# Optimization experiments

Measured on AMD Instinct MI355X. Metric: run time of the kernel, lower is better.

## Reference

```python
import jax, jax.numpy as jnp
import numpy as np

DIM = 256
HEADS = 4
DEPTH = DIM // HEADS
EXPAND = 4
EPS = 1e-3  # keras BatchNormalization default epsilon


def _bn(x, gamma, beta, mean, var):
    # inference-mode batch norm over last axis
    return gamma * (x - mean) * jax.lax.rsqrt(var + EPS) + beta


def setup_inputs() -> dict:
    key = jax.random.key(0)
    ks = jax.random.split(key, 12)
    B, S, D = 4, 2048, DIM
    H = D * EXPAND
    s = 1.0 / np.sqrt(D)
    inp = {
        "x": jax.random.normal(ks[0], (B, S, D), jnp.float32),
        "bn1_gamma": jnp.ones((D,), jnp.float32),
        "bn1_beta": jnp.zeros((D,), jnp.float32),
        "bn1_mean": jax.random.normal(ks[1], (D,), jnp.float32) * 0.1,
        "bn1_var": jnp.abs(jax.random.normal(ks[2], (D,), jnp.float32)) + 0.5,
        "wq": jax.random.normal(ks[3], (D, D), jnp.float32) * s,
        "bq": jnp.zeros((D,), jnp.float32),
        "wk": jax.random.normal(ks[4], (D, D), jnp.float32) * s,
        "bk": jnp.zeros((D,), jnp.float32),
        "wv": jax.random.normal(ks[5], (D, D), jnp.float32) * s,
        "bv": jnp.zeros((D,), jnp.float32),
        "wo": jax.random.normal(ks[6], (D, D), jnp.float32) * s,
        "bo": jnp.zeros((D,), jnp.float32),
        "bn2_gamma": jnp.ones((D,), jnp.float32),
        "bn2_beta": jnp.zeros((D,), jnp.float32),
        "bn2_mean": jax.random.normal(ks[7], (D,), jnp.float32) * 0.1,
        "bn2_var": jnp.abs(jax.random.normal(ks[8], (D,), jnp.float32)) + 0.5,
        "w1": jax.random.normal(ks[9], (D, H), jnp.float32) * s,
        "w2": jax.random.normal(ks[10], (H, D), jnp.float32) * (1.0 / np.sqrt(H)),
    }
    return inp


def reference(x, bn1_gamma, bn1_beta, bn1_mean, bn1_var,
              wq, bq, wk, bk, wv, bv, wo, bo,
              bn2_gamma, bn2_beta, bn2_mean, bn2_var, w1, w2):
    B, S, D = x.shape
    h = _bn(x, bn1_gamma, bn1_beta, bn1_mean, bn1_var)
    # project and split heads -> [B, H, S, depth]
    def heads(t):
        return t.reshape(B, S, HEADS, DEPTH).transpose(0, 2, 1, 3)
    q = heads(h @ wq + bq)
    k = heads(h @ wk + bk)
    v = heads(h @ wv + bv)
    scores = jnp.einsum("bhqd,bhkd->bhqk", q, k) / jnp.sqrt(jnp.float32(DEPTH))
    attn = jax.nn.softmax(scores, axis=-1)
    ctx = jnp.einsum("bhqk,bhkd->bhqd", attn, v)
    ctx = ctx.transpose(0, 2, 1, 3).reshape(B, S, D)
    attn_out = ctx @ wo + bo
    x1 = attn_out + x  # residual (dropout = identity at inference)
    h2 = _bn(x1, bn2_gamma, bn2_beta, bn2_mean, bn2_var)
    m = jax.nn.gelu(h2 @ w1, approximate=False) @ w2
    return m + x1
```

## Files before the change

### kernel.cpp

```cpp
#include <hip/hip_runtime.h>

typedef unsigned short u16;
typedef unsigned int u32;
typedef short short8 __attribute__((ext_vector_type(8)));
typedef float f32x4 __attribute__((ext_vector_type(4)));

#define EPS 1e-3f
#define C1F 0.18033688011112042f

static __device__ __forceinline__ u16 f2bf(float f) {
    u32 u = __float_as_uint(f);
    u += 0x7fffu + ((u >> 16) & 1u);
    return (u16)(u >> 16);
}
static __device__ __forceinline__ u32 pack_bf2(float a, float b) {
    u32 ua = __float_as_uint(a) + 0x8000u;
    u32 ub = __float_as_uint(b) + 0x8000u;
    return __builtin_amdgcn_perm(ub, ua, 0x07060302u);
}
static __device__ __forceinline__ void async_cp16(const void* g, void* l) {
    __builtin_amdgcn_global_load_lds(
        (const __attribute__((address_space(1))) unsigned int*)g,
        (__attribute__((address_space(3))) unsigned int*)l, 16, 0, 0);
}

__global__ void prep_kernel(const float* __restrict__ wq, const float* __restrict__ wk,
                            const float* __restrict__ wv, const float* __restrict__ wo,
                            const float* __restrict__ w1, const float* __restrict__ w2,
                            const float* __restrict__ bq, const float* __restrict__ bk,
                            const float* __restrict__ g1, const float* __restrict__ b1,
                            const float* __restrict__ m1, const float* __restrict__ v1,
                            const float* __restrict__ g2, const float* __restrict__ b2,
                            const float* __restrict__ m2, const float* __restrict__ v2,
                            u16* __restrict__ wqkT, u16* __restrict__ wvT,
                            u16* __restrict__ woT, u16* __restrict__ w1T,
                            u16* __restrict__ w2T, float* __restrict__ bqk,
                            float* __restrict__ bn1sc, float* __restrict__ bn1sh,
                            float* __restrict__ bn2sc, float* __restrict__ bn2sh) {
    int idx = blockIdx.x * 256 + threadIdx.x;
    if (idx < 131072) {
        int n = idx >> 8, k = idx & 255;
        float v = (n < 256) ? wq[k * 256 + n] : wk[k * 256 + (n - 256)] * C1F;
        wqkT[idx] = f2bf(v);
    } else if (idx < 196608) {
        int i = idx - 131072; int n = i >> 8, k = i & 255;
        wvT[i] = f2bf(wv[k * 256 + n]);
    } else if (idx < 262144) {
        int i = idx - 196608; int n = i >> 8, k = i & 255;
        woT[i] = f2bf(wo[k * 256 + n]);
    } else if (idx < 524288) {
        int i = idx - 262144; int n = i >> 8, k = i & 255;
        w1T[i] = f2bf(w1[k * 1024 + n]);
    } else if (idx < 786432) {
        int i = idx - 524288; int n = i >> 10, k = i & 1023;
        w2T[i] = f2bf(w2[k * 256 + n]);
    } else if (idx < 786944) {
        int i = idx - 786432;
        bqk[i] = (i < 256) ? bq[i] : bk[i - 256] * C1F;
    } else if (idx < 787200) {
        int i = idx - 786944;
        float sc = g1[i] * rsqrtf(v1[i] + EPS);
        bn1sc[i] = sc; bn1sh[i] = b1[i] - m1[i] * sc;
    } else if (idx < 787456) {
        int i = idx - 787200;
        float sc = g2[i] * rsqrtf(v2[i] + EPS);
        bn2sc[i] = sc; bn2sh[i] = b2[i] - m2[i] * sc;
    }
}

__global__ void bn1_kernel(const float* __restrict__ x, const float* __restrict__ sc,
                           const float* __restrict__ sh, u16* __restrict__ h) {
    int idx = blockIdx.x * 256 + threadIdx.x;
    int base = idx * 4;
    int c = base & 255;
    float4 xv = *(const float4*)(x + base);
    float4 s4 = *(const float4*)(sc + c);
    float4 h4 = *(const float4*)(sh + c);
    ushort4 pk;
    pk.x = f2bf(fmaf(xv.x, s4.x, h4.x));
    pk.y = f2bf(fmaf(xv.y, s4.y, h4.y));
    pk.z = f2bf(fmaf(xv.z, s4.z, h4.z));
    pk.w = f2bf(fmaf(xv.w, s4.w, h4.w));
    *(ushort4*)(h + base) = pk;
}

template <int EPI, int MT>
__global__ __launch_bounds__(256) void gemm_ws(
        const u16* __restrict__ A, const u16* __restrict__ Bt,
        int M, int N, int K,
        const float* __restrict__ bias, const float* __restrict__ resid,
        float* __restrict__ out_f32, u16* __restrict__ out_bf,
        const float* __restrict__ b2sc, const float* __restrict__ b2sh) {
    __shared__ u16 lds_b[64 * 256];
    const int t = threadIdx.x;
    const int w = t >> 6, lane = t & 63;
    const int l = lane & 15, Q = lane >> 4;
    const int m0 = blockIdx.x * (MT * 64);
    const int n0 = blockIdx.y * 64;

    f32x4 acc[MT][4];
#pragma unroll
    for (int mt = 0; mt < MT; ++mt)
#pragma unroll
        for (int nt = 0; nt < 4; ++nt) acc[mt][nt] = (f32x4){0.f, 0.f, 0.f, 0.f};

    for (int kc = 0; kc < K; kc += 256) {
        __syncthreads();
#pragma unroll
        for (int j = 0; j < 8; ++j) {
            int cw = (w * 8 + j) * 64 + lane;
            int r = cw >> 5;
            int cs = cw & 31;
            int c = (cs & 24) | ((cs & 7) ^ (r & 7));
            async_cp16(Bt + (size_t)(n0 + r) * K + kc + c * 8, (char*)lds_b + (w * 8 + j) * 1024);
        }
        __syncthreads();
#pragma unroll
        for (int kd = 0; kd < 8; ++kd) {
            short8 bfr[4];
#pragma unroll
            for (int nt = 0; nt < 4; ++nt) {
                int r = nt * 16 + l;
                int c = kd * 4 + Q;
                int slot = (c & 24) | ((c & 7) ^ (r & 7));
                bfr[nt] = *(const short8*)(lds_b + r * 256 + slot * 8);
            }
#pragma unroll
            for (int mt = 0; mt < MT; ++mt) {
                short8 afr = *(const short8*)(A + (size_t)(m0 + w * 16 * MT + mt * 16 + l) * K
                                              + kc + kd * 32 + Q * 8);
#pragma unroll
                for (int nt = 0; nt < 4; ++nt)
                    acc[mt][nt] = __builtin_amdgcn_mfma_f32_16x16x32_bf16(afr, bfr[nt], acc[mt][nt], 0, 0, 0);
            }
        }
    }

#pragma unroll
    for (int mt = 0; mt < MT; ++mt)
#pragma unroll
        for (int nt = 0; nt < 4; ++nt)
#pragma unroll
            for (int r = 0; r < 4; ++r) {
                int row = m0 + w * 16 * MT + mt * 16 + Q * 4 + r;
                int col = n0 + nt * 16 + l;
                float val = acc[mt][nt][r];
                size_t oidx = (size_t)row * N + col;
                if (EPI == 0) {
                    out_bf[oidx] = f2bf(val + bias[col]);
                } else if (EPI == 1) {
                    val += bias[col] + resid[oidx];
                    out_f32[oidx] = val;
                    out_bf[oidx] = f2bf(fmaf(val, b2sc[col], b2sh[col]));
                } else if (EPI == 2) {
                    float gl = 0.5f * val * (1.f + erff(val * 0.70710678118654752f));
                    out_bf[oidx] = f2bf(gl);
                } else {
                    out_f32[oidx] = val + resid[oidx];
                }
            }
}

__global__ __launch_bounds__(256) void gemm_bt4(
        const u16* __restrict__ A, const u16* __restrict__ Bt,
        int M, int N, int K,
        const float* __restrict__ bias, u16* __restrict__ out_bf) {
    __shared__ u16 lds_a[64][72];
    __shared__ u16 lds_b[64][72];
    const int t = threadIdx.x;
    const int wave = t >> 6, lane = t & 63;
    const int l = lane & 15, Q = lane >> 4;
    const int m0 = blockIdx.x * 64;
    const int n0 = blockIdx.y * 64;

    f32x4 acc[4];
#pragma unroll
    for (int nt = 0; nt < 4; ++nt) acc[nt] = (f32x4){0.f, 0.f, 0.f, 0.f};

    for (int k0 = 0; k0 < K; k0 += 64) {
        __syncthreads();
#pragma unroll
        for (int i = 0; i < 2; ++i) {
            int c = t + i * 256;
            int row = c >> 3, c8 = c & 7;
            *(uint4*)(&lds_a[row][c8 * 8]) =
                *(const uint4*)(A + (size_t)(m0 + row) * K + k0 + c8 * 8);
            *(uint4*)(&lds_b[row][c8 * 8]) =
                *(const uint4*)(Bt + (size_t)(n0 + row) * K + k0 + c8 * 8);
        }
        __syncthreads();
#pragma unroll
        for (int kd = 0; kd < 2; ++kd) {
            short8 afr = *(const short8*)(&lds_a[wave * 16 + l][kd * 32 + Q * 8]);
            short8 bfr[4];
#pragma unroll
            for (int nt = 0; nt < 4; ++nt)
                bfr[nt] = *(const short8*)(&lds_b[nt * 16 + l][kd * 32 + Q * 8]);
#pragma unroll
            for (int nt = 0; nt < 4; ++nt)
                acc[nt] = __builtin_amdgcn_mfma_f32_16x16x32_bf16(afr, bfr[nt], acc[nt], 0, 0, 0);
        }
    }
#pragma unroll
    for (int nt = 0; nt < 4; ++nt)
#pragma unroll
        for (int r = 0; r < 4; ++r) {
            int row = m0 + wave * 16 + Q * 4 + r;
            int col = n0 + nt * 16 + l;
            out_bf[(size_t)row * N + col] = f2bf(acc[nt][r] + bias[row]);
        }
}

static __device__ __forceinline__ void stage_tiles(const u16* kglob, const u16* vglob,
                                                   u16* kdst, u16* vdst,
                                                   int w, int lane, int kt) {
#pragma unroll
    for (int j = 0; j < 2; ++j) {
        int cw = (w * 2 + j) * 64 + lane;
        int r = cw >> 3;
        int c = (cw & 7) ^ (r & 7);
        async_cp16(kglob + ((size_t)(kt * 64 + r)) * 512 + c * 8, kdst + (w * 2 + j) * 512);
        async_cp16(vglob + ((size_t)r) * 8192 + kt * 64 + c * 8, vdst + (w * 2 + j) * 512);
    }
}

__global__ __launch_bounds__(256) void attn_kernel(const u16* __restrict__ qk,
                                                   const u16* __restrict__ vT,
                                                   float* __restrict__ opart,
                                                   float* __restrict__ lpart) {
    __shared__ u16 kbuf[2][4096];
    __shared__ u16 vbuf[2][4096];
    __shared__ u32 pbuf[8 * 16 * 36];
    const int t = threadIdx.x;
    const int w = t >> 6, lane = t & 63;
    const int l = lane & 15, Q = lane >> 4;
    const int qt = blockIdx.x;
    const int bh = blockIdx.y;
    const int sp = blockIdx.z;
    const int bb = bh >> 2, hd = bh & 3;
    const size_t rowbase = (size_t)bb * 2048;
    const int q0 = qt * 128 + w * 32;
    const int s_base = sp * 1024;

    short8 qf[2][2];
#pragma unroll
    for (int qg = 0; qg < 2; ++qg)
#pragma unroll
        for (int kd = 0; kd < 2; ++kd)
            qf[qg][kd] = *(const short8*)(qk + (rowbase + q0 + qg * 16 + l) * 512
                                          + hd * 64 + kd * 32 + Q * 8);

    f32x4 o[2][4];
#pragma unroll
    for (int qg = 0; qg < 2; ++qg)
#pragma unroll
        for (int dt = 0; dt < 4; ++dt) o[qg][dt] = (f32x4){0.f, 0.f, 0.f, 0.f};
    float lacc[2] = {0.f, 0.f};

    const u16* kglob = qk + (rowbase + s_base) * 512 + 256 + hd * 64;
    const u16* vglob = vT + ((size_t)(hd * 64)) * 8192 + rowbase + s_base;
    u32* pw = pbuf + w * 1152;

    stage_tiles(kglob, vglob, kbuf[0], vbuf[0], w, lane, 0);

    for (int kt = 0; kt < 16; ++kt) {
        __syncthreads();
        if (kt < 15)
            stage_tiles(kglob, vglob, kbuf[(kt + 1) & 1], vbuf[(kt + 1) & 1], w, lane, kt + 1);
        const u16* kb = kbuf[kt & 1];
        const u16* vb = vbuf[kt & 1];

#pragma unroll
        for (int st = 0; st < 4; ++st) {
            int r = st * 16 + l;
            short8 kf0 = *(const short8*)(kb + r * 64 + ((0 + Q) ^ (r & 7)) * 8);
            short8 kf1 = *(const short8*)(kb + r * 64 + ((4 + Q) ^ (r & 7)) * 8);
#pragma unroll
            for (int qg = 0; qg < 2; ++qg) {
                f32x4 s = (f32x4){0.f, 0.f, 0.f, 0.f};
                s = __builtin_amdgcn_mfma_f32_16x16x32_bf16(kf0, qf[qg][0], s, 0, 0, 0);
                s = __builtin_amdgcn_mfma_f32_16x16x32_bf16(kf1, qf[qg][1], s, 0, 0, 0);
                float p0 = exp2f(fminf(s[0], 100.f));
                float p1 = exp2f(fminf(s[1], 100.f));
                float p2 = exp2f(fminf(s[2], 100.f));
                float p3 = exp2f(fminf(s[3], 100.f));
                lacc[qg] += (p0 + p1) + (p2 + p3);
                u32 d0 = pack_bf2(p0, p1);
                u32 d1 = pack_bf2(p2, p3);
                *(uint2*)&pw[qg * 576 + l * 36 + st * 8 + Q * 2] = make_uint2(d0, d1);
            }
        }

#pragma unroll
        for (int cc = 0; cc < 2; ++cc) {
            short8 pf0 = *(const short8*)&pw[l * 36 + cc * 16 + Q * 4];
            short8 pf1 = *(const short8*)&pw[576 + l * 36 + cc * 16 + Q * 4];
#pragma unroll
            for (int dt = 0; dt < 4; ++dt) {
                int r = dt * 16 + l;
                short8 vf = *(const short8*)(vb + r * 64 + ((cc * 4 + Q) ^ (r & 7)) * 8);
                o[0][dt] = __builtin_amdgcn_mfma_f32_16x16x32_bf16(vf, pf0, o[0][dt], 0, 0, 0);
                o[1][dt] = __builtin_amdgcn_mfma_f32_16x16x32_bf16(vf, pf1, o[1][dt], 0, 0, 0);
            }
        }
    }

#pragma unroll
    for (int qg = 0; qg < 2; ++qg) {
        float v = lacc[qg];
        v += __shfl_xor(v, 16);
        v += __shfl_xor(v, 32);
        lacc[qg] = v;
    }
    float* ob = opart + (((size_t)sp * 16 + bh) * 2048 + q0) * 64;
#pragma unroll
    for (int qg = 0; qg < 2; ++qg)
#pragma unroll
        for (int dt = 0; dt < 4; ++dt)
            *(f32x4*)(ob + (size_t)(qg * 16 + l) * 64 + dt * 16 + Q * 4) = o[qg][dt];
    if (Q == 0) {
        size_t lb = ((size_t)sp * 16 + bh) * 2048 + q0;
        lpart[lb + l] = lacc[0];
        lpart[lb + 16 + l] = lacc[1];
    }
}

__global__ void combine_kernel(const float* __restrict__ opart,
                               const float* __restrict__ lpart,
                               u16* __restrict__ ctx) {
    int idx = blockIdx.x * 256 + threadIdx.x;
    int e = idx * 4;
    int row = e >> 8, col = e & 255;
    int b = row >> 11, s = row & 2047, h = col >> 6, d = col & 63;
    size_t pb = (((size_t)(b * 4 + h)) * 2048 + s) * 64 + d;
    f32x4 o1 = *(const f32x4*)(opart + pb);
    f32x4 o2 = *(const f32x4*)(opart + 2097152 + pb);
    size_t lb = (size_t)(b * 4 + h) * 2048 + s;
    float li = 1.0f / (lpart[lb] + lpart[32768 + lb]);
    ushort4 pk;
    pk.x = f2bf((o1[0] + o2[0]) * li);
    pk.y = f2bf((o1[1] + o2[1]) * li);
    pk.z = f2bf((o1[2] + o2[2]) * li);
    pk.w = f2bf((o1[3] + o2[3]) * li);
    *(ushort4*)(ctx + e) = pk;
}

extern "C" void kernel_launch(void* const* d_in, const int* in_sizes, int n_in,
                              void* d_out, int out_size, void* d_ws, size_t ws_size,
                              hipStream_t stream) {
    (void)in_sizes; (void)n_in; (void)out_size; (void)ws_size;
    const float* x  = (const float*)d_in[0];
    const float* g1 = (const float*)d_in[1];
    const float* b1 = (const float*)d_in[2];
    const float* m1 = (const float*)d_in[3];
    const float* v1 = (const float*)d_in[4];
    const float* wq = (const float*)d_in[5];
    const float* bq = (const float*)d_in[6];
    const float* wk = (const float*)d_in[7];
    const float* bk = (const float*)d_in[8];
    const float* wv = (const float*)d_in[9];
    const float* bv = (const float*)d_in[10];
    const float* wo = (const float*)d_in[11];
    const float* bo = (const float*)d_in[12];
    const float* g2 = (const float*)d_in[13];
    const float* b2 = (const float*)d_in[14];
    const float* m2 = (const float*)d_in[15];
    const float* v2 = (const float*)d_in[16];
    const float* w1 = (const float*)d_in[17];
    const float* w2 = (const float*)d_in[18];

    char* ws = (char*)d_ws;
    u16*   qkb   = (u16*)(ws + 0);
    u16*   ctxh  = (u16*)(ws + 8388608);
    float* x1    = (float*)(ws + 12582912);
    u16*   h2    = (u16*)(ws + 20971520);
    float* opart = (float*)(ws + 25165824);
    u16*   gbuf  = (u16*)(ws + 25165824);
    u16*   vTb   = (u16*)(ws + 41943040);
    u16*   wqkT  = (u16*)(ws + 46137344);
    u16*   wvT   = (u16*)(ws + 46399488);
    u16*   woT   = (u16*)(ws + 46530560);
    u16*   w1T   = (u16*)(ws + 46661632);
    u16*   w2T   = (u16*)(ws + 47185920);
    float* bqk   = (float*)(ws + 47710208);
    float* bn1sc = (float*)(ws + 47712256);
    float* bn1sh = (float*)(ws + 47713280);
    float* bn2sc = (float*)(ws + 47714304);
    float* bn2sh = (float*)(ws + 47715328);
    float* lpart = (float*)(ws + 12582912);
    u16*   h_buf = ctxh;
    u16*   ctx   = ctxh;
    float* out   = (float*)d_out;

    prep_kernel<<<3076, 256, 0, stream>>>(wq, wk, wv, wo, w1, w2, bq, bk,
                                          g1, b1, m1, v1, g2, b2, m2, v2,
                                          wqkT, wvT, woT, w1T, w2T, bqk,
                                          bn1sc, bn1sh, bn2sc, bn2sh);
    bn1_kernel<<<2048, 256, 0, stream>>>(x, bn1sc, bn1sh, h_buf);
    gemm_ws<0, 2><<<dim3(64, 8), 256, 0, stream>>>(
        h_buf, wqkT, 8192, 512, 256, bqk, nullptr, nullptr, qkb, nullptr, nullptr);
    gemm_bt4<<<dim3(4, 128), 256, 0, stream>>>(wvT, h_buf, 256, 8192, 256, bv, vTb);
    attn_kernel<<<dim3(16, 16, 2), 256, 0, stream>>>(qkb, vTb, opart, lpart);
    combine_kernel<<<2048, 256, 0, stream>>>(opart, lpart, ctx);
    gemm_ws<1, 1><<<dim3(128, 4), 256, 0, stream>>>(
        ctx, woT, 8192, 256, 256, bo, x, x1, h2, bn2sc, bn2sh);
    gemm_ws<2, 2><<<dim3(64, 16), 256, 0, stream>>>(
        h2, w1T, 8192, 1024, 256, nullptr, nullptr, nullptr, gbuf, nullptr, nullptr);
    gemm_ws<3, 1><<<dim3(128, 4), 256, 0, stream>>>(
        gbuf, w2T, 8192, 256, 1024, nullptr, x1, out, nullptr, nullptr, nullptr);
}
```

Measured before the change: 211.1 us.

## Fuse QKV projection, drop LDS in GEMMs, register-resident P, 4-way KV split

Merges the V projection into the QK GEMM, whose epilogue writes V transposed, so the separate gemm_bt4 launch is removed. GEMMs now load B fragments straight from global memory instead of staging them in LDS, which removes the barriers but may lose data reuse across waves. The attention kernel keeps softmax probabilities in registers and feeds them to 16x16x16 MFMAs instead of round-tripping through LDS. The KV split grows from 2 to 4 for more parallelism, with bf16 partial outputs that halve combine traffic at some precision cost.

```diff
diff --git a/kernel.cpp b/kernel.cpp
--- a/kernel.cpp
+++ b/kernel.cpp
@@ -3,16 +3,27 @@
 typedef unsigned short u16;
 typedef unsigned int u32;
 typedef short short8 __attribute__((ext_vector_type(8)));
+typedef short short4v __attribute__((ext_vector_type(4)));
 typedef float f32x4 __attribute__((ext_vector_type(4)));
 
 #define EPS 1e-3f
 #define C1F 0.18033688011112042f
+
+#if defined(__HIP_DEVICE_COMPILE__)
+#define MFMA16(a, b, c) __builtin_amdgcn_mfma_f32_16x16x16bf16_1k(a, b, c, 0, 0, 0)
+#else
+#define MFMA16(a, b, c) (c)
+#endif
 
 static __device__ __forceinline__ u16 f2bf(float f) {
     u32 u = __float_as_uint(f);
     u += 0x7fffu + ((u >> 16) & 1u);
     return (u16)(u >> 16);
 }
+static __device__ __forceinline__ float bf2f(u16 v) {
+    u32 u = (u32)v << 16;
+    return __uint_as_float(u);
+}
 static __device__ __forceinline__ u32 pack_bf2(float a, float b) {
     u32 ua = __float_as_uint(a) + 0x8000u;
     u32 ub = __float_as_uint(b) + 0x8000u;
@@ -28,23 +39,24 @@
                             const float* __restrict__ wv, const float* __restrict__ wo,
                             const float* __restrict__ w1, const float* __restrict__ w2,
                             const float* __restrict__ bq, const float* __restrict__ bk,
+                            const float* __restrict__ bv,
                             const float* __restrict__ g1, const float* __restrict__ b1,
                             const float* __restrict__ m1, const float* __restrict__ v1,
                             const float* __restrict__ g2, const float* __restrict__ b2,
                             const float* __restrict__ m2, const float* __restrict__ v2,
-                            u16* __restrict__ wqkT, u16* __restrict__ wvT,
-                            u16* __restrict__ woT, u16* __restrict__ w1T,
-                            u16* __restrict__ w2T, float* __restrict__ bqk,
+                            u16* __restrict__ wqkvT, u16* __restrict__ woT,
+                            u16* __restrict__ w1T, u16* __restrict__ w2T,
+                            float* __restrict__ bqkv,
                             float* __restrict__ bn1sc, float* __restrict__ bn1sh,
                             float* __restrict__ bn2sc, float* __restrict__ bn2sh) {
     int idx = blockIdx.x * 256 + threadIdx.x;
-    if (idx < 131072) {
+    if (idx < 196608) {
         int n = idx >> 8, k = idx & 255;
-        float v = (n < 256) ? wq[k * 256 + n] : wk[k * 256 + (n - 256)] * C1F;
-        wqkT[idx] = f2bf(v);
-    } else if (idx < 196608) {
-        int i = idx - 131072; int n = i >> 8, k = i & 255;
-        wvT[i] = f2bf(wv[k * 256 + n]);
+        float v;
+        if (n < 256)      v = wq[k * 256 + n];
+        else if (n < 512) v = wk[k * 256 + (n - 256)] * C1F;
+        else              v = wv[k * 256 + (n - 512)];
+        wqkvT[idx] = f2bf(v);
     } else if (idx < 262144) {
         int i = idx - 196608; int n = i >> 8, k = i & 255;
         woT[i] = f2bf(wo[k * 256 + n]);
@@ -54,15 +66,15 @@
     } else if (idx < 786432) {
         int i = idx - 524288; int n = i >> 10, k = i & 1023;
         w2T[i] = f2bf(w2[k * 256 + n]);
-    } else if (idx < 786944) {
+    } else if (idx < 787200) {
         int i = idx - 786432;
-        bqk[i] = (i < 256) ? bq[i] : bk[i - 256] * C1F;
-    } else if (idx < 787200) {
-        int i = idx - 786944;
+        bqkv[i] = (i < 256) ? bq[i] : (i < 512 ? bk[i - 256] * C1F : bv[i - 512]);
+    } else if (idx < 787456) {
+        int i = idx - 787200;
         float sc = g1[i] * rsqrtf(v1[i] + EPS);
         bn1sc[i] = sc; bn1sh[i] = b1[i] - m1[i] * sc;
-    } else if (idx < 787456) {
-        int i = idx - 787200;
+    } else if (idx < 787712) {
+        int i = idx - 787456;
         float sc = g2[i] * rsqrtf(v2[i] + EPS);
         bn2sc[i] = sc; bn2sh[i] = b2[i] - m2[i] * sc;
     }
@@ -85,129 +97,82 @@
 }
 
 template <int EPI, int MT>
-__global__ __launch_bounds__(256) void gemm_ws(
+__global__ __launch_bounds__(256) void gemm_nb(
         const u16* __restrict__ A, const u16* __restrict__ Bt,
         int M, int N, int K,
         const float* __restrict__ bias, const float* __restrict__ resid,
         float* __restrict__ out_f32, u16* __restrict__ out_bf,
+        u16* __restrict__ out_vt,
         const float* __restrict__ b2sc, const float* __restrict__ b2sh) {
-    __shared__ u16 lds_b[64 * 256];
     const int t = threadIdx.x;
     const int w = t >> 6, lane = t & 63;
     const int l = lane & 15, Q = lane >> 4;
-    const int m0 = blockIdx.x * (MT * 64);
+    const int m0 = blockIdx.x * (MT * 64) + w * (MT * 16);
     const int n0 = blockIdx.y * 64;
 
+    const u16* Ab = A + (size_t)(m0 + l) * K + Q * 8;
+    const u16* Bb = Bt + (size_t)(n0 + l) * K + Q * 8;
+
     f32x4 acc[MT][4];
 #pragma unroll
     for (int mt = 0; mt < MT; ++mt)
 #pragma unroll
         for (int nt = 0; nt < 4; ++nt) acc[mt][nt] = (f32x4){0.f, 0.f, 0.f, 0.f};
 
-    for (int kc = 0; kc < K; kc += 256) {
-        __syncthreads();
-#pragma unroll
-        for (int j = 0; j < 8; ++j) {
-            int cw = (w * 8 + j) * 64 + lane;
-            int r = cw >> 5;
-            int cs = cw & 31;
-            int c = (cs & 24) | ((cs & 7) ^ (r & 7));
-            async_cp16(Bt + (size_t)(n0 + r) * K + kc + c * 8, (char*)lds_b + (w * 8 + j) * 1024);
-        }
-        __syncthreads();
-#pragma unroll
-        for (int kd = 0; kd < 8; ++kd) {
-            short8 bfr[4];
-#pragma unroll
-            for (int nt = 0; nt < 4; ++nt) {
-                int r = nt * 16 + l;
-                int c = kd * 4 + Q;
-                int slot = (c & 24) | ((c & 7) ^ (r & 7));
-                bfr[nt] = *(const short8*)(lds_b + r * 256 + slot * 8);
-            }
-#pragma unroll
-            for (int mt = 0; mt < MT; ++mt) {
-                short8 afr = *(const short8*)(A + (size_t)(m0 + w * 16 * MT + mt * 16 + l) * K
-                                              + kc + kd * 32 + Q * 8);
-#pragma unroll
-                for (int nt = 0; nt < 4; ++nt)
-                    acc[mt][nt] = __builtin_amdgcn_mfma_f32_16x16x32_bf16(afr, bfr[nt], acc[mt][nt], 0, 0, 0);
-            }
+    const int K32 = K >> 5;
+#pragma unroll 4
+    for (int kd = 0; kd < K32; ++kd) {
+        short8 bfr[4];
+#pragma unroll
+        for (int nt = 0; nt < 4; ++nt)
+            bfr[nt] = *(const short8*)(Bb + (size_t)(nt * 16) * K + kd * 32);
+#pragma unroll
+        for (int mt = 0; mt < MT; ++mt) {
+            short8 afr = *(const short8*)(Ab + (size_t)(mt * 16) * K + kd * 32);
+#pragma unroll
+            for (int nt = 0; nt < 4; ++nt)
+                acc[mt][nt] = __builtin_amdgcn_mfma_f32_16x16x32_bf16(afr, bfr[nt], acc[mt][nt], 0, 0, 0);
         }
     }
 
 #pragma unroll
     for (int mt = 0; mt < MT; ++mt)
 #pragma unroll
-        for (int nt = 0; nt < 4; ++nt)
-#pragma unroll
-            for (int r = 0; r < 4; ++r) {
-                int row = m0 + w * 16 * MT + mt * 16 + Q * 4 + r;
-                int col = n0 + nt * 16 + l;
-                float val = acc[mt][nt][r];
-                size_t oidx = (size_t)row * N + col;
-                if (EPI == 0) {
-                    out_bf[oidx] = f2bf(val + bias[col]);
-                } else if (EPI == 1) {
-                    val += bias[col] + resid[oidx];
-                    out_f32[oidx] = val;
-                    out_bf[oidx] = f2bf(fmaf(val, b2sc[col], b2sh[col]));
-                } else if (EPI == 2) {
-                    float gl = 0.5f * val * (1.f + erff(val * 0.70710678118654752f));
-                    out_bf[oidx] = f2bf(gl);
+        for (int nt = 0; nt < 4; ++nt) {
+            int col = n0 + nt * 16 + l;
+            int row0 = m0 + mt * 16 + Q * 4;
+            if (EPI == 0) {
+                float b = bias[col];
+                if (col < 512) {
+#pragma unroll
+                    for (int r = 0; r < 4; ++r)
+                        out_bf[(size_t)(row0 + r) * 512 + col] = f2bf(acc[mt][nt][r] + b);
                 } else {
-                    out_f32[oidx] = val + resid[oidx];
+                    ushort4 pk;
+                    pk.x = f2bf(acc[mt][nt][0] + b);
+                    pk.y = f2bf(acc[mt][nt][1] + b);
+                    pk.z = f2bf(acc[mt][nt][2] + b);
+                    pk.w = f2bf(acc[mt][nt][3] + b);
+                    *(ushort4*)(out_vt + (size_t)(col - 512) * 8192 + row0) = pk;
+                }
+            } else {
+#pragma unroll
+                for (int r = 0; r < 4; ++r) {
+                    int row = row0 + r;
+                    float val = acc[mt][nt][r];
+                    size_t oidx = (size_t)row * N + col;
+                    if (EPI == 1) {
+                        val += bias[col] + resid[oidx];
+                        out_f32[oidx] = val;
+                        out_bf[oidx] = f2bf(fmaf(val, b2sc[col], b2sh[col]));
+                    } else if (EPI == 2) {
+                        float gl = 0.5f * val * (1.f + erff(val * 0.70710678118654752f));
+                        out_bf[oidx] = f2bf(gl);
+                    } else {
+                        out_f32[oidx] = val + resid[oidx];
+                    }
                 }
             }
-}
-
-__global__ __launch_bounds__(256) void gemm_bt4(
-        const u16* __restrict__ A, const u16* __restrict__ Bt,
-        int M, int N, int K,
-        const float* __restrict__ bias, u16* __restrict__ out_bf) {
-    __shared__ u16 lds_a[64][72];
-    __shared__ u16 lds_b[64][72];
-    const int t = threadIdx.x;
-    const int wave = t >> 6, lane = t & 63;
-    const int l = lane & 15, Q = lane >> 4;
-    const int m0 = blockIdx.x * 64;
-    const int n0 = blockIdx.y * 64;
-
-    f32x4 acc[4];
-#pragma unroll
-    for (int nt = 0; nt < 4; ++nt) acc[nt] = (f32x4){0.f, 0.f, 0.f, 0.f};
-
-    for (int k0 = 0; k0 < K; k0 += 64) {
-        __syncthreads();
-#pragma unroll
-        for (int i = 0; i < 2; ++i) {
-            int c = t + i * 256;
-            int row = c >> 3, c8 = c & 7;
-            *(uint4*)(&lds_a[row][c8 * 8]) =
-                *(const uint4*)(A + (size_t)(m0 + row) * K + k0 + c8 * 8);
-            *(uint4*)(&lds_b[row][c8 * 8]) =
-                *(const uint4*)(Bt + (size_t)(n0 + row) * K + k0 + c8 * 8);
-        }
-        __syncthreads();
-#pragma unroll
-        for (int kd = 0; kd < 2; ++kd) {
-            short8 afr = *(const short8*)(&lds_a[wave * 16 + l][kd * 32 + Q * 8]);
-            short8 bfr[4];
-#pragma unroll
-            for (int nt = 0; nt < 4; ++nt)
-                bfr[nt] = *(const short8*)(&lds_b[nt * 16 + l][kd * 32 + Q * 8]);
-#pragma unroll
-            for (int nt = 0; nt < 4; ++nt)
-                acc[nt] = __builtin_amdgcn_mfma_f32_16x16x32_bf16(afr, bfr[nt], acc[nt], 0, 0, 0);
-        }
-    }
-#pragma unroll
-    for (int nt = 0; nt < 4; ++nt)
-#pragma unroll
-        for (int r = 0; r < 4; ++r) {
-            int row = m0 + wave * 16 + Q * 4 + r;
-            int col = n0 + nt * 16 + l;
-            out_bf[(size_t)row * N + col] = f2bf(acc[nt][r] + bias[row]);
         }
 }
 
@@ -226,11 +191,10 @@
 
 __global__ __launch_bounds__(256) void attn_kernel(const u16* __restrict__ qk,
                                                    const u16* __restrict__ vT,
-                                                   float* __restrict__ opart,
+                                                   u16* __restrict__ opart,
                                                    float* __restrict__ lpart) {
     __shared__ u16 kbuf[2][4096];
     __shared__ u16 vbuf[2][4096];
-    __shared__ u32 pbuf[8 * 16 * 36];
     const int t = threadIdx.x;
     const int w = t >> 6, lane = t & 63;
     const int l = lane & 15, Q = lane >> 4;
@@ -240,7 +204,6 @@
     const int bb = bh >> 2, hd = bh & 3;
     const size_t rowbase = (size_t)bb * 2048;
     const int q0 = qt * 128 + w * 32;
-    const int s_base = sp * 1024;
 
     short8 qf[2][2];
 #pragma unroll
@@ -257,23 +220,23 @@
         for (int dt = 0; dt < 4; ++dt) o[qg][dt] = (f32x4){0.f, 0.f, 0.f, 0.f};
     float lacc[2] = {0.f, 0.f};
 
-    const u16* kglob = qk + (rowbase + s_base) * 512 + 256 + hd * 64;
-    const u16* vglob = vT + ((size_t)(hd * 64)) * 8192 + rowbase + s_base;
-    u32* pw = pbuf + w * 1152;
+    const u16* kglob = qk + (rowbase + sp * 512) * 512 + 256 + hd * 64;
+    const u16* vglob = vT + ((size_t)(hd * 64)) * 8192 + rowbase + sp * 512;
 
     stage_tiles(kglob, vglob, kbuf[0], vbuf[0], w, lane, 0);
 
-    for (int kt = 0; kt < 16; ++kt) {
+    for (int kt = 0; kt < 8; ++kt) {
         __syncthreads();
-        if (kt < 15)
+        if (kt < 7)
             stage_tiles(kglob, vglob, kbuf[(kt + 1) & 1], vbuf[(kt + 1) & 1], w, lane, kt + 1);
         const u16* kb = kbuf[kt & 1];
         const u16* vb = vbuf[kt & 1];
 
+        union { u32 u[2]; short4v s4; } pf[2][4];
 #pragma unroll
         for (int st = 0; st < 4; ++st) {
             int r = st * 16 + l;
-            short8 kf0 = *(const short8*)(kb + r * 64 + ((0 + Q) ^ (r & 7)) * 8);
+            short8 kf0 = *(const short8*)(kb + r * 64 + ((Q) ^ (r & 7)) * 8);
             short8 kf1 = *(const short8*)(kb + r * 64 + ((4 + Q) ^ (r & 7)) * 8);
 #pragma unroll
             for (int qg = 0; qg < 2; ++qg) {
@@ -285,22 +248,20 @@
                 float p2 = exp2f(fminf(s[2], 100.f));
                 float p3 = exp2f(fminf(s[3], 100.f));
                 lacc[qg] += (p0 + p1) + (p2 + p3);
-                u32 d0 = pack_bf2(p0, p1);
-                u32 d1 = pack_bf2(p2, p3);
-                *(uint2*)&pw[qg * 576 + l * 36 + st * 8 + Q * 2] = make_uint2(d0, d1);
+                pf[qg][st].u[0] = pack_bf2(p0, p1);
+                pf[qg][st].u[1] = pack_bf2(p2, p3);
             }
         }
 
 #pragma unroll
-        for (int cc = 0; cc < 2; ++cc) {
-            short8 pf0 = *(const short8*)&pw[l * 36 + cc * 16 + Q * 4];
-            short8 pf1 = *(const short8*)&pw[576 + l * 36 + cc * 16 + Q * 4];
+        for (int c = 0; c < 4; ++c) {
 #pragma unroll
             for (int dt = 0; dt < 4; ++dt) {
                 int r = dt * 16 + l;
-                short8 vf = *(const short8*)(vb + r * 64 + ((cc * 4 + Q) ^ (r & 7)) * 8);
-                o[0][dt] = __builtin_amdgcn_mfma_f32_16x16x32_bf16(vf, pf0, o[0][dt], 0, 0, 0);
-                o[1][dt] = __builtin_amdgcn_mfma_f32_16x16x32_bf16(vf, pf1, o[1][dt], 0, 0, 0);
+                int slot = (2 * c + (Q >> 1)) ^ (r & 7);
+                short4v vf = *(const short4v*)(vb + r * 64 + slot * 8 + (Q & 1) * 4);
+                o[0][dt] = MFMA16(vf, pf[0][c].s4, o[0][dt]);
+                o[1][dt] = MFMA16(vf, pf[1][c].s4, o[1][dt]);
             }
         }
     }
@@ -312,12 +273,18 @@
         v += __shfl_xor(v, 32);
         lacc[qg] = v;
     }
-    float* ob = opart + (((size_t)sp * 16 + bh) * 2048 + q0) * 64;
+    u16* ob = opart + (((size_t)sp * 16 + bh) * 2048 + q0) * 64;
 #pragma unroll
     for (int qg = 0; qg < 2; ++qg)
 #pragma unroll
-        for (int dt = 0; dt < 4; ++dt)
-            *(f32x4*)(ob + (size_t)(qg * 16 + l) * 64 + dt * 16 + Q * 4) = o[qg][dt];
+        for (int dt = 0; dt < 4; ++dt) {
+            ushort4 pk;
+            pk.x = f2bf(o[qg][dt][0]);
+            pk.y = f2bf(o[qg][dt][1]);
+            pk.z = f2bf(o[qg][dt][2]);
+            pk.w = f2bf(o[qg][dt][3]);
+            *(ushort4*)(ob + (size_t)(qg * 16 + l) * 64 + dt * 16 + Q * 4) = pk;
+        }
     if (Q == 0) {
         size_t lb = ((size_t)sp * 16 + bh) * 2048 + q0;
         lpart[lb + l] = lacc[0];
@@ -325,23 +292,27 @@
     }
 }
 
-__global__ void combine_kernel(const float* __restrict__ opart,
+__global__ void combine_kernel(const u16* __restrict__ opart,
                                const float* __restrict__ lpart,
                                u16* __restrict__ ctx) {
     int idx = blockIdx.x * 256 + threadIdx.x;
     int e = idx * 4;
     int row = e >> 8, col = e & 255;
     int b = row >> 11, s = row & 2047, h = col >> 6, d = col & 63;
-    size_t pb = (((size_t)(b * 4 + h)) * 2048 + s) * 64 + d;
-    f32x4 o1 = *(const f32x4*)(opart + pb);
-    f32x4 o2 = *(const f32x4*)(opart + 2097152 + pb);
-    size_t lb = (size_t)(b * 4 + h) * 2048 + s;
-    float li = 1.0f / (lpart[lb] + lpart[32768 + lb]);
+    float a0 = 0.f, a1 = 0.f, a2 = 0.f, a3 = 0.f, lsum = 0.f;
+#pragma unroll
+    for (int sp = 0; sp < 4; ++sp) {
+        size_t pb = (((size_t)sp * 16 + b * 4 + h) * 2048 + s) * 64 + d;
+        ushort4 ov = *(const ushort4*)(opart + pb);
+        a0 += bf2f(ov.x); a1 += bf2f(ov.y); a2 += bf2f(ov.z); a3 += bf2f(ov.w);
+        lsum += lpart[((size_t)sp * 16 + b * 4 + h) * 2048 + s];
+    }
+    float li = 1.0f / lsum;
     ushort4 pk;
-    pk.x = f2bf((o1[0] + o2[0]) * li);
-    pk.y = f2bf((o1[1] + o2[1]) * li);
-    pk.z = f2bf((o1[2] + o2[2]) * li);
-    pk.w = f2bf((o1[3] + o2[3]) * li);
+    pk.x = f2bf(a0 * li);
+    pk.y = f2bf(a1 * li);
+    pk.z = f2bf(a2 * li);
+    pk.w = f2bf(a3 * li);
     *(ushort4*)(ctx + e) = pk;
 }
 
@@ -370,42 +341,40 @@
     const float* w2 = (const float*)d_in[18];
 
     char* ws = (char*)d_ws;
-    u16*   qkb   = (u16*)(ws + 0);
-    u16*   ctxh  = (u16*)(ws + 8388608);
-    float* x1    = (float*)(ws + 12582912);
-    u16*   h2    = (u16*)(ws + 20971520);
-    float* opart = (float*)(ws + 25165824);
-    u16*   gbuf  = (u16*)(ws + 25165824);
-    u16*   vTb   = (u16*)(ws + 41943040);
-    u16*   wqkT  = (u16*)(ws + 46137344);
-    u16*   wvT   = (u16*)(ws + 46399488);
-    u16*   woT   = (u16*)(ws + 46530560);
-    u16*   w1T   = (u16*)(ws + 46661632);
-    u16*   w2T   = (u16*)(ws + 47185920);
-    float* bqk   = (float*)(ws + 47710208);
-    float* bn1sc = (float*)(ws + 47712256);
-    float* bn1sh = (float*)(ws + 47713280);
-    float* bn2sc = (float*)(ws + 47714304);
-    float* bn2sh = (float*)(ws + 47715328);
-    float* lpart = (float*)(ws + 12582912);
-    u16*   h_buf = ctxh;
-    u16*   ctx   = ctxh;
-    float* out   = (float*)d_out;
-
-    prep_kernel<<<3076, 256, 0, stream>>>(wq, wk, wv, wo, w1, w2, bq, bk,
+    u16*   qkb    = (u16*)(ws + 0);
+    u16*   ctxh   = (u16*)(ws + 8388608);
+    float* x1     = (float*)(ws + 12582912);
+    float* lpart  = (float*)(ws + 12582912);
+    u16*   h2     = (u16*)(ws + 20971520);
+    u16*   opart  = (u16*)(ws + 25165824);
+    u16*   gbuf   = (u16*)(ws + 25165824);
+    u16*   vTb    = (u16*)(ws + 41943040);
+    u16*   wqkvT  = (u16*)(ws + 46137344);
+    u16*   woT    = (u16*)(ws + 46530560);
+    u16*   w1T    = (u16*)(ws + 46661632);
+    u16*   w2T    = (u16*)(ws + 47185920);
+    float* bqkv   = (float*)(ws + 47710208);
+    float* bn1sc  = (float*)(ws + 47713280);
+    float* bn1sh  = (float*)(ws + 47714304);
+    float* bn2sc  = (float*)(ws + 47715328);
+    float* bn2sh  = (float*)(ws + 47716352);
+    u16*   h_buf  = ctxh;
+    u16*   ctx    = ctxh;
+    float* out    = (float*)d_out;
+
+    prep_kernel<<<3077, 256, 0, stream>>>(wq, wk, wv, wo, w1, w2, bq, bk, bv,
                                           g1, b1, m1, v1, g2, b2, m2, v2,
-                                          wqkT, wvT, woT, w1T, w2T, bqk,
+                                          wqkvT, woT, w1T, w2T, bqkv,
                                           bn1sc, bn1sh, bn2sc, bn2sh);
     bn1_kernel<<<2048, 256, 0, stream>>>(x, bn1sc, bn1sh, h_buf);
-    gemm_ws<0, 2><<<dim3(64, 8), 256, 0, stream>>>(
-        h_buf, wqkT, 8192, 512, 256, bqk, nullptr, nullptr, qkb, nullptr, nullptr);
-    gemm_bt4<<<dim3(4, 128), 256, 0, stream>>>(wvT, h_buf, 256, 8192, 256, bv, vTb);
-    attn_kernel<<<dim3(16, 16, 2), 256, 0, stream>>>(qkb, vTb, opart, lpart);
+    gemm_nb<0, 2><<<dim3(64, 12), 256, 0, stream>>>(
+        h_buf, wqkvT, 8192, 768, 256, bqkv, nullptr, nullptr, qkb, vTb, nullptr, nullptr);
+    attn_kernel<<<dim3(16, 16, 4), 256, 0, stream>>>(qkb, vTb, opart, lpart);
     combine_kernel<<<2048, 256, 0, stream>>>(opart, lpart, ctx);
-    gemm_ws<1, 1><<<dim3(128, 4), 256, 0, stream>>>(
-        ctx, woT, 8192, 256, 256, bo, x, x1, h2, bn2sc, bn2sh);
-    gemm_ws<2, 2><<<dim3(64, 16), 256, 0, stream>>>(
-        h2, w1T, 8192, 1024, 256, nullptr, nullptr, nullptr, gbuf, nullptr, nullptr);
-    gemm_ws<3, 1><<<dim3(128, 4), 256, 0, stream>>>(
-        gbuf, w2T, 8192, 256, 1024, nullptr, x1, out, nullptr, nullptr, nullptr);
-}
+    gemm_nb<1, 1><<<dim3(128, 4), 256, 0, stream>>>(
+        ctx, woT, 8192, 256, 256, bo, x, x1, h2, nullptr, bn2sc, bn2sh);
+    gemm_nb<2, 2><<<dim3(64, 16), 256, 0, stream>>>(
+        h2, w1T, 8192, 1024, 256, nullptr, nullptr, nullptr, gbuf, nullptr, nullptr, nullptr);
+    gemm_nb<3, 1><<<dim3(128, 4), 256, 0, stream>>>(
+        gbuf, w2T, 8192, 256, 1024, nullptr, x1, out, nullptr, nullptr, nullptr, nullptr);
+}
```

Result: slower. 244.2 us (+15.7%).
